# Kernel tuning notes

Measured on AMD Instinct MI355X. Metric: run time of the kernel, lower is better.

The kernel has to match this reference:

```python
import jax, jax.numpy as jnp
import numpy as np

D = 512      # n_embd
H = 8        # n_head
L = 2        # n_layer (per stack)
T = 2048     # sequence length / block_size
B = 1        # batch
BANDS = (999, 9)  # band_width for [phase, tool] stacks
EPS = 1e-5


def _sinusoidal(n_pos, dim):
    pos = np.arange(n_pos)[:, None].astype(np.float64)
    j = np.arange(dim)[None, :]
    angle = pos / np.power(10000.0, 2 * (j // 2) / dim)
    out = np.zeros((n_pos, dim), np.float32)
    out[:, 0::2] = np.sin(angle[:, 0::2])
    out[:, 1::2] = np.cos(angle[:, 1::2])
    return jnp.asarray(out)


def setup_inputs() -> dict:
    key = jax.random.key(0)
    ks = jax.random.split(key, 8)
    s = 0.02
    rn = lambda k, shp: jax.random.normal(k, shp, jnp.float32) * s
    inp = {
        "x": jax.random.normal(ks[0], (B, T, D), jnp.float32),
        "pos_emb": _sinusoidal(T, D),            # sinusoidal, frozen
        # leading dim 2 = [phase stack, tool stack], then layer dim L
        "ln1_w": jnp.ones((2, L, D)), "ln1_b": jnp.zeros((2, L, D)),
        "ln2_w": jnp.ones((2, L, D)), "ln2_b": jnp.zeros((2, L, D)),
        "Wq": rn(ks[1], (2, L, D, D)), "bq": jnp.zeros((2, L, D)),
        "Wk": rn(ks[2], (2, L, D, D)), "bk": jnp.zeros((2, L, D)),
        "Wv": rn(ks[3], (2, L, D, D)), "bv": jnp.zeros((2, L, D)),
        "Wo": rn(ks[4], (2, L, D, D)), "bo": jnp.zeros((2, L, D)),
        "W1": rn(ks[5], (2, L, D, 2 * D)), "b1": jnp.zeros((2, L, 2 * D)),
        "W2": rn(ks[6], (2, L, 2 * D, D)), "b2": jnp.zeros((2, L, D)),
        "lnf_w": jnp.ones((D,)), "lnf_b": jnp.zeros((D,)),
    }
    return inp


def _ln(x, w, b):
    mu = x.mean(-1, keepdims=True)
    var = ((x - mu) ** 2).mean(-1, keepdims=True)
    return (x - mu) / jnp.sqrt(var + EPS) * w + b


def _attn(x, Wq, bq, Wk, bk, Wv, bv, Wo, bo, bw):
    Bx, Tx, _ = x.shape
    Dh = D // H
    heads = lambda W, b: (x @ W + b).reshape(Bx, Tx, H, Dh).transpose(0, 2, 1, 3)
    q, k, v = heads(Wq, bq), heads(Wk, bk), heads(Wv, bv)
    att = jnp.einsum('bhqd,bhkd->bhqk', q, k) / jnp.sqrt(jnp.float32(Dh))
    i = jnp.arange(Tx)[:, None]
    j = jnp.arange(Tx)[None, :]
    mask = (j <= i) & (j >= i - bw)  # causal band
    att = jnp.where(mask, att, -jnp.inf)
    att = jax.nn.softmax(att, axis=-1)
    y = jnp.einsum('bhqk,bhkd->bhqd', att, v).transpose(0, 2, 1, 3).reshape(Bx, Tx, D)
    return y @ Wo + bo


def reference(x, pos_emb, ln1_w, ln1_b, ln2_w, ln2_b,
              Wq, bq, Wk, bk, Wv, bv, Wo, bo,
              W1, b1, W2, b2, lnf_w, lnf_b):
    Tx = x.shape[1]
    h0 = x + pos_emb[None, :Tx]
    outs = []
    for s in range(2):  # phase stack, tool stack
        bw = BANDS[s]
        h = h0
        for l in range(L):
            h = h + _attn(_ln(h, ln1_w[s, l], ln1_b[s, l]),
                          Wq[s, l], bq[s, l], Wk[s, l], bk[s, l],
                          Wv[s, l], bv[s, l], Wo[s, l], bo[s, l], bw)
            hm = _ln(h, ln2_w[s, l], ln2_b[s, l])
            h = h + (jax.nn.gelu(hm @ W1[s, l] + b1[s, l], approximate=False)
                     @ W2[s, l] + b2[s, l])
        outs.append(_ln(h, lnf_w, lnf_b))
    return (outs[0], outs[1])
```

## Files before the change

### kernel.cpp

```cpp
#include <hip/hip_runtime.h>
#include <stdint.h>

#define T 2048
#define D 512
#define NH 8
#define DH 64
#define L 2

typedef float floatx4 __attribute__((ext_vector_type(4)));
typedef short shortx8 __attribute__((ext_vector_type(8)));
typedef unsigned short u16;
typedef unsigned short u16x4 __attribute__((ext_vector_type(4)));

__device__ __forceinline__ u16 f2bf(float f) {
    union { float f; uint32_t u; } c; c.f = f;
    uint32_t u = c.u;
    u += 0x7fffu + ((u >> 16) & 1u);
    return (u16)(u >> 16);
}

__device__ __forceinline__ void load_lds16(const void* g, void* l) {
    __builtin_amdgcn_global_load_lds((const __attribute__((address_space(1))) void*)g,
                                     (__attribute__((address_space(3))) void*)l,
                                     16, 0, 0);
}

struct TransJobs {
    const float* src[6];
    u16* dst[6];
    const float* x;
    const float* pos;
    float* h;
};

__global__ __launch_bounds__(256) void pre_kernel(TransJobs j) {
    __shared__ float tile[32][33];
    int tid = threadIdx.x;
    if (blockIdx.z == 24) {
        int idx = (blockIdx.y * 32 + blockIdx.x) * 256 + tid;
        float4 xv = ((const float4*)j.x)[idx];
        float4 pv = ((const float4*)j.pos)[idx];
        float4 r;
        r.x = xv.x + pv.x; r.y = xv.y + pv.y; r.z = xv.z + pv.z; r.w = xv.w + pv.w;
        ((float4*)j.h)[idx] = r;
        ((float4*)j.h)[idx + (T * D / 4)] = r;
        return;
    }
    int m = blockIdx.z >> 2, slice = blockIdx.z & 3;
    int R = (m == 5) ? 1024 : 512;
    int C = (m == 4) ? 1024 : 512;
    if (blockIdx.x * 32 >= C || blockIdx.y * 32 >= R) return;
    const float* in = j.src[m] + (size_t)slice * R * C;
    u16* out = j.dst[m] + (size_t)slice * R * C;
    int tx = tid & 31, ty = tid >> 5;
    int x = blockIdx.x * 32 + tx;
    int y0 = blockIdx.y * 32;
#pragma unroll
    for (int i = 0; i < 4; i++)
        tile[ty + i * 8][tx] = in[(size_t)(y0 + ty + i * 8) * C + x];
    __syncthreads();
    int ox = y0 + tx;
#pragma unroll
    for (int i = 0; i < 4; i++)
        out[(size_t)(blockIdx.x * 32 + ty + i * 8) * R + ox] = f2bf(tile[tx][ty + i * 8]);
}

__global__ __launch_bounds__(256) void ln_res_kernel(float* __restrict__ h,
                                                     const float* __restrict__ part,
                                                     const float* __restrict__ w0,
                                                     const float* __restrict__ b0,
                                                     u16* __restrict__ out, int l) {
    int row = blockIdx.x * 4 + (threadIdx.x >> 6);
    int lane = threadIdx.x & 63;
    int s = row >> 11;
    int c0 = lane * 4;
    float* xr = h + (size_t)row * D;
    float4 v0 = *(const float4*)(xr + c0);
    float4 v1 = *(const float4*)(xr + c0 + 256);
    if (part) {
        const float* p0r = part + (size_t)s * 2 * T * D + (size_t)(row & (T - 1)) * D;
        const float* p1r = p0r + (size_t)T * D;
        float4 a0 = *(const float4*)(p0r + c0), a1 = *(const float4*)(p0r + c0 + 256);
        float4 e0 = *(const float4*)(p1r + c0), e1 = *(const float4*)(p1r + c0 + 256);
        v0.x += a0.x + e0.x; v0.y += a0.y + e0.y; v0.z += a0.z + e0.z; v0.w += a0.w + e0.w;
        v1.x += a1.x + e1.x; v1.y += a1.y + e1.y; v1.z += a1.z + e1.z; v1.w += a1.w + e1.w;
        *(float4*)(xr + c0) = v0;
        *(float4*)(xr + c0 + 256) = v1;
    }
    float sum = v0.x + v0.y + v0.z + v0.w + v1.x + v1.y + v1.z + v1.w;
    float sq = v0.x*v0.x + v0.y*v0.y + v0.z*v0.z + v0.w*v0.w
             + v1.x*v1.x + v1.y*v1.y + v1.z*v1.z + v1.w*v1.w;
#pragma unroll
    for (int d2 = 1; d2 < 64; d2 <<= 1) { sum += __shfl_xor(sum, d2); sq += __shfl_xor(sq, d2); }
    float mu = sum * (1.0f / D);
    float var = sq * (1.0f / D) - mu * mu;
    float rstd = rsqrtf(var + 1e-5f);
    const float* w = w0 + (size_t)(s * L + l) * D;
    const float* b = b0 + (size_t)(s * L + l) * D;
    u16x4 p0, p1;
#pragma unroll
    for (int jj = 0; jj < 4; jj++) {
        float a = (jj == 0 ? v0.x : jj == 1 ? v0.y : jj == 2 ? v0.z : v0.w);
        p0[jj] = f2bf((a - mu) * rstd * w[c0 + jj] + b[c0 + jj]);
        float c = (jj == 0 ? v1.x : jj == 1 ? v1.y : jj == 2 ? v1.z : v1.w);
        p1[jj] = f2bf((c - mu) * rstd * w[c0 + 256 + jj] + b[c0 + 256 + jj]);
    }
    *(u16x4*)(out + (size_t)row * D + c0) = p0;
    *(u16x4*)(out + (size_t)row * D + c0 + 256) = p1;
}

__global__ __launch_bounds__(256) void lnf_kernel(const float* __restrict__ h,
                                                  const float* __restrict__ part,
                                                  const float* __restrict__ w,
                                                  const float* __restrict__ b,
                                                  float* __restrict__ out) {
    int row = blockIdx.x * 4 + (threadIdx.x >> 6);
    int lane = threadIdx.x & 63;
    int s = row >> 11;
    int c0 = lane * 4;
    const float* xr = h + (size_t)row * D;
    float4 v0 = *(const float4*)(xr + c0);
    float4 v1 = *(const float4*)(xr + c0 + 256);
    const float* p0r = part + (size_t)s * 2 * T * D + (size_t)(row & (T - 1)) * D;
    const float* p1r = p0r + (size_t)T * D;
    float4 a0 = *(const float4*)(p0r + c0), a1 = *(const float4*)(p0r + c0 + 256);
    float4 e0 = *(const float4*)(p1r + c0), e1 = *(const float4*)(p1r + c0 + 256);
    v0.x += a0.x + e0.x; v0.y += a0.y + e0.y; v0.z += a0.z + e0.z; v0.w += a0.w + e0.w;
    v1.x += a1.x + e1.x; v1.y += a1.y + e1.y; v1.z += a1.z + e1.z; v1.w += a1.w + e1.w;
    float sum = v0.x + v0.y + v0.z + v0.w + v1.x + v1.y + v1.z + v1.w;
    float sq = v0.x*v0.x + v0.y*v0.y + v0.z*v0.z + v0.w*v0.w
             + v1.x*v1.x + v1.y*v1.y + v1.z*v1.z + v1.w*v1.w;
#pragma unroll
    for (int d2 = 1; d2 < 64; d2 <<= 1) { sum += __shfl_xor(sum, d2); sq += __shfl_xor(sq, d2); }
    float mu = sum * (1.0f / D);
    float var = sq * (1.0f / D) - mu * mu;
    float rstd = rsqrtf(var + 1e-5f);
    float4 r0, r1;
    r0.x = (v0.x - mu) * rstd * w[c0+0] + b[c0+0];
    r0.y = (v0.y - mu) * rstd * w[c0+1] + b[c0+1];
    r0.z = (v0.z - mu) * rstd * w[c0+2] + b[c0+2];
    r0.w = (v0.w - mu) * rstd * w[c0+3] + b[c0+3];
    r1.x = (v1.x - mu) * rstd * w[c0+256+0] + b[c0+256+0];
    r1.y = (v1.y - mu) * rstd * w[c0+256+1] + b[c0+256+1];
    r1.z = (v1.z - mu) * rstd * w[c0+256+2] + b[c0+256+2];
    r1.w = (v1.w - mu) * rstd * w[c0+256+3] + b[c0+256+3];
    *(float4*)(out + (size_t)row * D + c0) = r0;
    *(float4*)(out + (size_t)row * D + c0 + 256) = r1;
}

struct GemmPtrs {
    const u16* A[6];
    const u16* Bt[6];
    const float* bias[6];
    void* C[6];
};

#define EPI_QKV  0
#define EPI_GELU 1
#define EPI_PART 2

template <int EPI>
__global__ __launch_bounds__(256) void gemm_kernel(GemmPtrs p, int M, int N, int K, int KS) {
    __shared__ __align__(16) u16 lA[2][128 * 32];
    __shared__ __align__(16) u16 lB[2][64 * 32];
    int nchunk = K / KS;
    int pidx = blockIdx.z / nchunk;
    int kc = blockIdx.z % nchunk;
    int koff = kc * KS;
    const u16* A = p.A[pidx];
    const u16* Bt = p.Bt[pidx];
    int m0 = blockIdx.y * 128, n0 = blockIdx.x * 64;
    int tid = threadIdx.x;
    int lane = tid & 63, wave = tid >> 6;
    int wx = wave & 1, wy = wave >> 1;
    int l16 = lane & 15, q4 = lane >> 4;
    const u16* ag = A + (size_t)(m0 + (tid >> 2)) * K + koff + (tid & 3) * 8;
    const u16* bg = Bt + (size_t)(n0 + (tid >> 2)) * K + koff + (tid & 3) * 8;
    size_t rowskip = (size_t)64 * K;
    floatx4 acc[4][2] = {};
    for (int k0 = 0; k0 < KS; k0 += 64) {
        __syncthreads();
#pragma unroll
        for (int kh = 0; kh < 2; kh++) {
            load_lds16(ag + k0 + kh * 32, &lA[kh][tid * 8]);
            load_lds16(ag + rowskip + k0 + kh * 32, &lA[kh][64 * 32 + tid * 8]);
            load_lds16(bg + k0 + kh * 32, &lB[kh][tid * 8]);
        }
        __syncthreads();
#pragma unroll
        for (int kh = 0; kh < 2; kh++) {
            shortx8 af[4], bf[2];
#pragma unroll
            for (int t = 0; t < 4; t++)
                af[t] = *(const shortx8*)(&lA[kh][(wy * 64 + t * 16 + l16) * 32 + q4 * 8]);
#pragma unroll
            for (int t = 0; t < 2; t++)
                bf[t] = *(const shortx8*)(&lB[kh][(wx * 32 + t * 16 + l16) * 32 + q4 * 8]);
#pragma unroll
            for (int i = 0; i < 4; i++)
#pragma unroll
                for (int j = 0; j < 2; j++)
                    acc[i][j] = __builtin_amdgcn_mfma_f32_16x16x32_bf16(af[i], bf[j], acc[i][j], 0, 0, 0);
        }
    }
    const float* bias = p.bias[pidx];
    bool vtrans = (EPI == EPI_QKV) && (pidx % 3 == 2);
#pragma unroll
    for (int i = 0; i < 4; i++) {
        int row0 = m0 + wy * 64 + i * 16 + q4 * 4;
#pragma unroll
        for (int j = 0; j < 2; j++) {
            int col = n0 + wx * 32 + j * 16 + l16;
            float bz = (kc == 0) ? bias[col] : 0.0f;
            floatx4 a = acc[i][j];
            if (EPI == EPI_QKV) {
                if (vtrans) {
                    u16x4 pk;
#pragma unroll
                    for (int r = 0; r < 4; r++) pk[r] = f2bf(a[r] + bz);
                    *(u16x4*)((u16*)p.C[pidx] + (size_t)col * M + row0) = pk;
                } else {
#pragma unroll
                    for (int r = 0; r < 4; r++)
                        ((u16*)p.C[pidx])[(size_t)(row0 + r) * N + col] = f2bf(a[r] + bz);
                }
            } else if (EPI == EPI_GELU) {
#pragma unroll
                for (int r = 0; r < 4; r++) {
                    float v = a[r] + bz;
                    float g = 0.5f * v * (1.0f + erff(v * 0.70710678118f));
                    ((u16*)p.C[pidx])[(size_t)(row0 + r) * N + col] = f2bf(g);
                }
            } else {
#pragma unroll
                for (int r = 0; r < 4; r++)
                    ((float*)p.C[pidx])[(size_t)kc * M * N + (size_t)(row0 + r) * N + col] = a[r] + bz;
            }
        }
    }
}

__global__ __launch_bounds__(256) void attn_kernel(const u16* __restrict__ qg,
                                                   const u16* __restrict__ kg,
                                                   const u16* __restrict__ vtg,
                                                   u16* __restrict__ ao,
                                                   int bw0, int bw1) {
    __shared__ __align__(16) u16 pbuf[4][16 * 32];
    __shared__ float cm[4][16], cl[4][16];
    __shared__ float co[4][16][64];
    int s = blockIdx.z, hh = blockIdx.y, q0 = blockIdx.x * 16;
    int bw = (s == 0) ? bw0 : bw1;
    int tid = threadIdx.x, wave = tid >> 6, lane = tid & 63;
    int l16 = lane & 15, q4 = lane >> 4;
    const u16* Q = qg + (size_t)s * T * D;
    const u16* Kp = kg + (size_t)s * T * D;
    const u16* V = vtg + (size_t)s * D * T;
    int hd = hh * DH;
    shortx8 qf0 = *(const shortx8*)(Q + (size_t)(q0 + l16) * D + hd + q4 * 8);
    shortx8 qf1 = *(const shortx8*)(Q + (size_t)(q0 + l16) * D + hd + 32 + q4 * 8);
    floatx4 o[4] = {};
    float m[4], lsum[4];
#pragma unroll
    for (int r = 0; r < 4; r++) { m[r] = -3e38f; lsum[r] = 0.0f; }
    int klo = q0 - bw; if (klo < 0) klo = 0; klo &= ~31;
    int khi = q0 + 15;
    u16* pw = pbuf[wave];
    for (int kt = klo + wave * 32; kt <= khi; kt += 128) {
        floatx4 s0 = {}, s1 = {};
        {
            shortx8 kf0 = *(const shortx8*)(Kp + (size_t)(kt + l16) * D + hd + q4 * 8);
            shortx8 kf1 = *(const shortx8*)(Kp + (size_t)(kt + l16) * D + hd + 32 + q4 * 8);
            s0 = __builtin_amdgcn_mfma_f32_16x16x32_bf16(qf0, kf0, s0, 0, 0, 0);
            s0 = __builtin_amdgcn_mfma_f32_16x16x32_bf16(qf1, kf1, s0, 0, 0, 0);
            shortx8 kf2 = *(const shortx8*)(Kp + (size_t)(kt + 16 + l16) * D + hd + q4 * 8);
            shortx8 kf3 = *(const shortx8*)(Kp + (size_t)(kt + 16 + l16) * D + hd + 32 + q4 * 8);
            s1 = __builtin_amdgcn_mfma_f32_16x16x32_bf16(qf0, kf2, s1, 0, 0, 0);
            s1 = __builtin_amdgcn_mfma_f32_16x16x32_bf16(qf1, kf3, s1, 0, 0, 0);
        }
        float al[4];
#pragma unroll
        for (int r = 0; r < 4; r++) {
            int row = q0 + q4 * 4 + r;
            int c0 = kt + l16, c1 = kt + 16 + l16;
            float sv0 = (c0 <= row && c0 >= row - bw) ? s0[r] * 0.125f : -3e38f;
            float sv1 = (c1 <= row && c1 >= row - bw) ? s1[r] * 0.125f : -3e38f;
            float tmax = fmaxf(sv0, sv1);
#pragma unroll
            for (int d2 = 1; d2 < 16; d2 <<= 1) tmax = fmaxf(tmax, __shfl_xor(tmax, d2));
            float mnew = fmaxf(m[r], tmax);
            float a = __expf(m[r] - mnew);
            float p0 = (sv0 > -1e37f) ? __expf(sv0 - mnew) : 0.0f;
            float p1 = (sv1 > -1e37f) ? __expf(sv1 - mnew) : 0.0f;
            float ps = p0 + p1;
#pragma unroll
            for (int d2 = 1; d2 < 16; d2 <<= 1) ps += __shfl_xor(ps, d2);
            lsum[r] = lsum[r] * a + ps;
            m[r] = mnew;
            al[r] = a;
            pw[(q4 * 4 + r) * 32 + l16] = f2bf(p0);
            pw[(q4 * 4 + r) * 32 + 16 + l16] = f2bf(p1);
        }
#pragma unroll
        for (int n = 0; n < 4; n++)
#pragma unroll
            for (int r = 0; r < 4; r++) o[n][r] *= al[r];
        shortx8 pf = *(const shortx8*)(pw + l16 * 32 + q4 * 8);
#pragma unroll
        for (int n = 0; n < 4; n++) {
            shortx8 vf = *(const shortx8*)(V + (size_t)(hd + n * 16 + l16) * T + kt + q4 * 8);
            o[n] = __builtin_amdgcn_mfma_f32_16x16x32_bf16(pf, vf, o[n], 0, 0, 0);
        }
    }
    if (l16 == 0) {
#pragma unroll
        for (int r = 0; r < 4; r++) {
            cm[wave][q4 * 4 + r] = m[r];
            cl[wave][q4 * 4 + r] = lsum[r];
        }
    }
#pragma unroll
    for (int n = 0; n < 4; n++)
#pragma unroll
        for (int r = 0; r < 4; r++)
            co[wave][q4 * 4 + r][n * 16 + l16] = o[n][r];
    __syncthreads();
#pragma unroll
    for (int i = 0; i < 4; i++) {
        int idx = tid + i * 256;
        int row = idx >> 6, col = idx & 63;
        float M = fmaxf(fmaxf(cm[0][row], cm[1][row]), fmaxf(cm[2][row], cm[3][row]));
        float Ls = 0.0f, O = 0.0f;
#pragma unroll
        for (int w = 0; w < 4; w++) {
            float e = __expf(cm[w][row] - M);
            Ls += cl[w][row] * e;
            O += co[w][row][col] * e;
        }
        ao[(size_t)s * T * D + (size_t)(q0 + row) * D + hd + col] = f2bf(O / Ls);
    }
}

extern "C" void kernel_launch(void* const* d_in, const int* in_sizes, int n_in,
                              void* d_out, int out_size, void* d_ws, size_t ws_size,
                              hipStream_t stream) {
    (void)in_sizes; (void)n_in; (void)out_size; (void)ws_size;
    const float* x     = (const float*)d_in[0];
    const float* pos   = (const float*)d_in[1];
    const float* ln1_w = (const float*)d_in[2];
    const float* ln1_b = (const float*)d_in[3];
    const float* ln2_w = (const float*)d_in[4];
    const float* ln2_b = (const float*)d_in[5];
    const float* Wq    = (const float*)d_in[6];
    const float* bq    = (const float*)d_in[7];
    const float* Wk    = (const float*)d_in[8];
    const float* bk    = (const float*)d_in[9];
    const float* Wv    = (const float*)d_in[10];
    const float* bv    = (const float*)d_in[11];
    const float* Wo    = (const float*)d_in[12];
    const float* bo    = (const float*)d_in[13];
    const float* W1    = (const float*)d_in[14];
    const float* b1    = (const float*)d_in[15];
    const float* W2    = (const float*)d_in[16];
    const float* b2    = (const float*)d_in[17];
    const float* lnf_w = (const float*)d_in[18];
    const float* lnf_b = (const float*)d_in[19];

    char* ws = (char*)d_ws;
    size_t off = 0;
    auto alloc = [&](size_t bytes) { void* p = ws + off; off += (bytes + 255) & ~(size_t)255; return p; };
    u16* WqT = (u16*)alloc((size_t)4 * 512 * 512 * 2);
    u16* WkT = (u16*)alloc((size_t)4 * 512 * 512 * 2);
    u16* WvT = (u16*)alloc((size_t)4 * 512 * 512 * 2);
    u16* WoT = (u16*)alloc((size_t)4 * 512 * 512 * 2);
    u16* W1T = (u16*)alloc((size_t)4 * 512 * 1024 * 2);
    u16* W2T = (u16*)alloc((size_t)4 * 1024 * 512 * 2);
    float* h = (float*)alloc((size_t)2 * T * D * 4);
    u16* xln = (u16*)alloc((size_t)2 * T * D * 2);
    u16* qb  = (u16*)alloc((size_t)2 * T * D * 2);
    u16* kb  = (u16*)alloc((size_t)2 * T * D * 2);
    u16* vt  = (u16*)alloc((size_t)2 * T * D * 2);
    u16* ao  = (u16*)alloc((size_t)2 * T * D * 2);
    u16* ff  = (u16*)alloc((size_t)2 * T * 1024 * 2);
    float* pp = (float*)alloc((size_t)2 * 2 * T * D * 4);
    float* pf = (float*)alloc((size_t)2 * 2 * T * D * 4);

    TransJobs tj;
    tj.src[0] = Wq; tj.dst[0] = WqT;
    tj.src[1] = Wk; tj.dst[1] = WkT;
    tj.src[2] = Wv; tj.dst[2] = WvT;
    tj.src[3] = Wo; tj.dst[3] = WoT;
    tj.src[4] = W1; tj.dst[4] = W1T;
    tj.src[5] = W2; tj.dst[5] = W2T;
    tj.x = x; tj.pos = pos; tj.h = h;
    pre_kernel<<<dim3(32, 32, 25), 256, 0, stream>>>(tj);

    for (int l = 0; l < L; l++) {
        ln_res_kernel<<<(2 * T) / 4, 256, 0, stream>>>(h, l == 0 ? nullptr : pf,
                                                       ln1_w, ln1_b, xln, l);

        GemmPtrs g{};
        for (int s = 0; s < 2; s++) {
            int wo = s * L + l;
            const u16* a = xln + (size_t)s * T * D;
            g.A[s * 3 + 0] = a; g.Bt[s * 3 + 0] = WqT + (size_t)wo * 512 * 512;
            g.bias[s * 3 + 0] = bq + (size_t)wo * 512; g.C[s * 3 + 0] = qb + (size_t)s * T * D;
            g.A[s * 3 + 1] = a; g.Bt[s * 3 + 1] = WkT + (size_t)wo * 512 * 512;
            g.bias[s * 3 + 1] = bk + (size_t)wo * 512; g.C[s * 3 + 1] = kb + (size_t)s * T * D;
            g.A[s * 3 + 2] = a; g.Bt[s * 3 + 2] = WvT + (size_t)wo * 512 * 512;
            g.bias[s * 3 + 2] = bv + (size_t)wo * 512; g.C[s * 3 + 2] = vt + (size_t)s * T * D;
        }
        gemm_kernel<EPI_QKV><<<dim3(8, 16, 6), 256, 0, stream>>>(g, T, 512, 512, 512);

        attn_kernel<<<dim3(128, 8, 2), 256, 0, stream>>>(qb, kb, vt, ao, 999, 9);

        GemmPtrs gp{};
        for (int s = 0; s < 2; s++) {
            int wo = s * L + l;
            gp.A[s] = ao + (size_t)s * T * D;
            gp.Bt[s] = WoT + (size_t)wo * 512 * 512;
            gp.bias[s] = bo + (size_t)wo * 512;
            gp.C[s] = pp + (size_t)s * 2 * T * D;
        }
        gemm_kernel<EPI_PART><<<dim3(8, 16, 4), 256, 0, stream>>>(gp, T, 512, 512, 256);

        ln_res_kernel<<<(2 * T) / 4, 256, 0, stream>>>(h, pp, ln2_w, ln2_b, xln, l);

        GemmPtrs g1{};
        for (int s = 0; s < 2; s++) {
            int wo = s * L + l;
            g1.A[s] = xln + (size_t)s * T * D;
            g1.Bt[s] = W1T + (size_t)wo * 512 * 1024;
            g1.bias[s] = b1 + (size_t)wo * 1024;
            g1.C[s] = ff + (size_t)s * T * 1024;
        }
        gemm_kernel<EPI_GELU><<<dim3(16, 16, 2), 256, 0, stream>>>(g1, T, 1024, 512, 512);

        GemmPtrs g2{};
        for (int s = 0; s < 2; s++) {
            int wo = s * L + l;
            g2.A[s] = ff + (size_t)s * T * 1024;
            g2.Bt[s] = W2T + (size_t)wo * 1024 * 512;
            g2.bias[s] = b2 + (size_t)wo * 512;
            g2.C[s] = pf + (size_t)s * 2 * T * D;
        }
        gemm_kernel<EPI_PART><<<dim3(8, 16, 4), 256, 0, stream>>>(g2, T, 512, 1024, 512);
    }

    lnf_kernel<<<(2 * T) / 4, 256, 0, stream>>>(h, pf, lnf_w, lnf_b, (float*)d_out);
}
```

Baseline: 342.9 us.

## Load GEMM fragments directly from global and store split-K partials as bf16

The GEMM drops its LDS staging (global_load_lds plus two barriers per K step) and has each wave load its MFMA fragments straight from global memory, relying on cache for reuse across waves. Split-K partial outputs are also written as bf16 instead of fp32, halving the traffic for the partial buffers read by the residual/LayerNorm kernels. The risks are more uncoalesced global reads and lost data reuse in the GEMM, plus reduced precision in the residual partial sums.

Measured after the change: 437.2 us. 27.5% more time.

```diff
diff --git a/kernel.cpp b/kernel.cpp
--- a/kernel.cpp
+++ b/kernel.cpp
@@ -19,10 +19,9 @@
     return (u16)(u >> 16);
 }
 
-__device__ __forceinline__ void load_lds16(const void* g, void* l) {
-    __builtin_amdgcn_global_load_lds((const __attribute__((address_space(1))) void*)g,
-                                     (__attribute__((address_space(3))) void*)l,
-                                     16, 0, 0);
+__device__ __forceinline__ float bf2f(u16 v) {
+    union { uint32_t u; float f; } c; c.u = ((uint32_t)v) << 16;
+    return c.f;
 }
 
 struct TransJobs {
@@ -66,7 +65,7 @@
 }
 
 __global__ __launch_bounds__(256) void ln_res_kernel(float* __restrict__ h,
-                                                     const float* __restrict__ part,
+                                                     const u16* __restrict__ part,
                                                      const float* __restrict__ w0,
                                                      const float* __restrict__ b0,
                                                      u16* __restrict__ out, int l) {
@@ -78,12 +77,14 @@
     float4 v0 = *(const float4*)(xr + c0);
     float4 v1 = *(const float4*)(xr + c0 + 256);
     if (part) {
-        const float* p0r = part + (size_t)s * 2 * T * D + (size_t)(row & (T - 1)) * D;
-        const float* p1r = p0r + (size_t)T * D;
-        float4 a0 = *(const float4*)(p0r + c0), a1 = *(const float4*)(p0r + c0 + 256);
-        float4 e0 = *(const float4*)(p1r + c0), e1 = *(const float4*)(p1r + c0 + 256);
-        v0.x += a0.x + e0.x; v0.y += a0.y + e0.y; v0.z += a0.z + e0.z; v0.w += a0.w + e0.w;
-        v1.x += a1.x + e1.x; v1.y += a1.y + e1.y; v1.z += a1.z + e1.z; v1.w += a1.w + e1.w;
+        const u16* p0r = part + (size_t)s * 2 * T * D + (size_t)(row & (T - 1)) * D;
+        const u16* p1r = p0r + (size_t)T * D;
+        u16x4 a0 = *(const u16x4*)(p0r + c0), a1 = *(const u16x4*)(p0r + c0 + 256);
+        u16x4 e0 = *(const u16x4*)(p1r + c0), e1 = *(const u16x4*)(p1r + c0 + 256);
+        v0.x += bf2f(a0[0]) + bf2f(e0[0]); v0.y += bf2f(a0[1]) + bf2f(e0[1]);
+        v0.z += bf2f(a0[2]) + bf2f(e0[2]); v0.w += bf2f(a0[3]) + bf2f(e0[3]);
+        v1.x += bf2f(a1[0]) + bf2f(e1[0]); v1.y += bf2f(a1[1]) + bf2f(e1[1]);
+        v1.z += bf2f(a1[2]) + bf2f(e1[2]); v1.w += bf2f(a1[3]) + bf2f(e1[3]);
         *(float4*)(xr + c0) = v0;
         *(float4*)(xr + c0 + 256) = v1;
     }
@@ -110,7 +111,7 @@
 }
 
 __global__ __launch_bounds__(256) void lnf_kernel(const float* __restrict__ h,
-                                                  const float* __restrict__ part,
+                                                  const u16* __restrict__ part,
                                                   const float* __restrict__ w,
                                                   const float* __restrict__ b,
                                                   float* __restrict__ out) {
@@ -121,12 +122,14 @@
     const float* xr = h + (size_t)row * D;
     float4 v0 = *(const float4*)(xr + c0);
     float4 v1 = *(const float4*)(xr + c0 + 256);
-    const float* p0r = part + (size_t)s * 2 * T * D + (size_t)(row & (T - 1)) * D;
-    const float* p1r = p0r + (size_t)T * D;
-    float4 a0 = *(const float4*)(p0r + c0), a1 = *(const float4*)(p0r + c0 + 256);
-    float4 e0 = *(const float4*)(p1r + c0), e1 = *(const float4*)(p1r + c0 + 256);
-    v0.x += a0.x + e0.x; v0.y += a0.y + e0.y; v0.z += a0.z + e0.z; v0.w += a0.w + e0.w;
-    v1.x += a1.x + e1.x; v1.y += a1.y + e1.y; v1.z += a1.z + e1.z; v1.w += a1.w + e1.w;
+    const u16* p0r = part + (size_t)s * 2 * T * D + (size_t)(row & (T - 1)) * D;
+    const u16* p1r = p0r + (size_t)T * D;
+    u16x4 a0 = *(const u16x4*)(p0r + c0), a1 = *(const u16x4*)(p0r + c0 + 256);
+    u16x4 e0 = *(const u16x4*)(p1r + c0), e1 = *(const u16x4*)(p1r + c0 + 256);
+    v0.x += bf2f(a0[0]) + bf2f(e0[0]); v0.y += bf2f(a0[1]) + bf2f(e0[1]);
+    v0.z += bf2f(a0[2]) + bf2f(e0[2]); v0.w += bf2f(a0[3]) + bf2f(e0[3]);
+    v1.x += bf2f(a1[0]) + bf2f(e1[0]); v1.y += bf2f(a1[1]) + bf2f(e1[1]);
+    v1.z += bf2f(a1[2]) + bf2f(e1[2]); v1.w += bf2f(a1[3]) + bf2f(e1[3]);
     float sum = v0.x + v0.y + v0.z + v0.w + v1.x + v1.y + v1.z + v1.w;
     float sq = v0.x*v0.x + v0.y*v0.y + v0.z*v0.z + v0.w*v0.w
              + v1.x*v1.x + v1.y*v1.y + v1.z*v1.z + v1.w*v1.w;
@@ -161,8 +164,6 @@
 
 template <int EPI>
 __global__ __launch_bounds__(256) void gemm_kernel(GemmPtrs p, int M, int N, int K, int KS) {
-    __shared__ __align__(16) u16 lA[2][128 * 32];
-    __shared__ __align__(16) u16 lB[2][64 * 32];
     int nchunk = K / KS;
     int pidx = blockIdx.z / nchunk;
     int kc = blockIdx.z % nchunk;
@@ -174,34 +175,23 @@
     int lane = tid & 63, wave = tid >> 6;
     int wx = wave & 1, wy = wave >> 1;
     int l16 = lane & 15, q4 = lane >> 4;
-    const u16* ag = A + (size_t)(m0 + (tid >> 2)) * K + koff + (tid & 3) * 8;
-    const u16* bg = Bt + (size_t)(n0 + (tid >> 2)) * K + koff + (tid & 3) * 8;
-    size_t rowskip = (size_t)64 * K;
+    const u16* arow = A + (size_t)(m0 + wy * 64 + l16) * K + koff + q4 * 8;
+    const u16* brow = Bt + (size_t)(n0 + wx * 32 + l16) * K + koff + q4 * 8;
     floatx4 acc[4][2] = {};
-    for (int k0 = 0; k0 < KS; k0 += 64) {
-        __syncthreads();
-#pragma unroll
-        for (int kh = 0; kh < 2; kh++) {
-            load_lds16(ag + k0 + kh * 32, &lA[kh][tid * 8]);
-            load_lds16(ag + rowskip + k0 + kh * 32, &lA[kh][64 * 32 + tid * 8]);
-            load_lds16(bg + k0 + kh * 32, &lB[kh][tid * 8]);
-        }
-        __syncthreads();
-#pragma unroll
-        for (int kh = 0; kh < 2; kh++) {
-            shortx8 af[4], bf[2];
-#pragma unroll
-            for (int t = 0; t < 4; t++)
-                af[t] = *(const shortx8*)(&lA[kh][(wy * 64 + t * 16 + l16) * 32 + q4 * 8]);
-#pragma unroll
-            for (int t = 0; t < 2; t++)
-                bf[t] = *(const shortx8*)(&lB[kh][(wx * 32 + t * 16 + l16) * 32 + q4 * 8]);
-#pragma unroll
-            for (int i = 0; i < 4; i++)
-#pragma unroll
-                for (int j = 0; j < 2; j++)
-                    acc[i][j] = __builtin_amdgcn_mfma_f32_16x16x32_bf16(af[i], bf[j], acc[i][j], 0, 0, 0);
-        }
+#pragma unroll 2
+    for (int k0 = 0; k0 < KS; k0 += 32) {
+        shortx8 af[4], bf[2];
+#pragma unroll
+        for (int t = 0; t < 4; t++)
+            af[t] = *(const shortx8*)(arow + (size_t)(t * 16) * K + k0);
+#pragma unroll
+        for (int t = 0; t < 2; t++)
+            bf[t] = *(const shortx8*)(brow + (size_t)(t * 16) * K + k0);
+#pragma unroll
+        for (int i = 0; i < 4; i++)
+#pragma unroll
+            for (int j = 0; j < 2; j++)
+                acc[i][j] = __builtin_amdgcn_mfma_f32_16x16x32_bf16(af[i], bf[j], acc[i][j], 0, 0, 0);
     }
     const float* bias = p.bias[pidx];
     bool vtrans = (EPI == EPI_QKV) && (pidx % 3 == 2);
@@ -234,7 +224,7 @@
             } else {
 #pragma unroll
                 for (int r = 0; r < 4; r++)
-                    ((float*)p.C[pidx])[(size_t)kc * M * N + (size_t)(row0 + r) * N + col] = a[r] + bz;
+                    ((u16*)p.C[pidx])[(size_t)kc * M * N + (size_t)(row0 + r) * N + col] = f2bf(a[r] + bz);
             }
         }
     }
@@ -381,8 +371,8 @@
     u16* vt  = (u16*)alloc((size_t)2 * T * D * 2);
     u16* ao  = (u16*)alloc((size_t)2 * T * D * 2);
     u16* ff  = (u16*)alloc((size_t)2 * T * 1024 * 2);
-    float* pp = (float*)alloc((size_t)2 * 2 * T * D * 4);
-    float* pf = (float*)alloc((size_t)2 * 2 * T * D * 4);
+    u16* pp = (u16*)alloc((size_t)2 * 2 * T * D * 2);
+    u16* pf = (u16*)alloc((size_t)2 * 2 * T * D * 2);
 
     TransJobs tj;
     tj.src[0] = Wq; tj.dst[0] = WqT;
```
